# Kernel tuning notes

Measured on AMD Instinct MI355X. Metric: run time of the kernel, lower is better.

## Reference

```python
import jax, jax.numpy as jnp
import numpy as np

N_NODES = 50000


def gcn_layer(h, src, dst, W, b):
    # h: [N, Fin] -> [N, Fout]; symmetric-normalized aggregation with self-loops
    h = h @ W
    n = h.shape[0]
    deg = jnp.zeros((n,), h.dtype).at[dst].add(1.0) + 1.0  # +1 for self-loop
    dinv = jax.lax.rsqrt(deg)
    msg = h[src] * dinv[src, None]                      # gather + scale by src norm
    agg = jax.ops.segment_sum(msg, dst, num_segments=n) # scatter-add at dst
    agg = agg * dinv[:, None]                           # scale by dst norm
    agg = agg + h * (dinv * dinv)[:, None]              # self-loop contribution
    return agg + b


def setup_inputs() -> dict:
    key = jax.random.key(0)
    ks = jax.random.split(key, 8)
    G, N, E, F = 8, N_NODES, 800000, 128
    x = jax.random.normal(ks[0], (G, N, F), dtype=jnp.float32)
    edge_index = jax.random.randint(ks[1], (G, 2, E), 0, N, dtype=jnp.int64)
    s = 1.0 / np.sqrt(F)
    W0 = jax.random.normal(ks[2], (F, F), dtype=jnp.float32) * s
    W1 = jax.random.normal(ks[3], (F, F), dtype=jnp.float32) * s
    W2 = jax.random.normal(ks[4], (F, F), dtype=jnp.float32) * s
    b0 = jnp.zeros((F,), jnp.float32)
    b1 = jnp.zeros((F,), jnp.float32)
    b2 = jnp.zeros((F,), jnp.float32)
    return {"x": x, "edge_index": edge_index, "W0": W0, "b0": b0,
            "W1": W1, "b1": b1, "W2": W2, "b2": b2}


def reference(x, edge_index, W0, b0, W1, b1, W2, b2):
    # dropout is identity in eval mode; relu applied after every layer
    def per_graph(xg, eg):
        src, dst = eg[0], eg[1]
        h = xg
        for W, b in ((W0, b0), (W1, b1), (W2, b2)):
            h = jax.nn.relu(gcn_layer(h, src, dst, W, b))
        return h
    return jax.vmap(per_graph)(x, edge_index)  # [G, N, output_dim]
```

## Files before the change

### kernel.cpp

```cpp
#include <hip/hip_runtime.h>

constexpr int G    = 8;
constexpr int NN   = 50000;
constexpr int EE   = 800000;
constexpr int F    = 128;
constexpr int NBK  = (NN + 255) / 256;
constexpr int CAP2 = 4608;
constexpr int CHA  = 8192;
constexpr int NBA  = (EE + CHA - 1) / CHA;

typedef float  float4_t __attribute__((ext_vector_type(4)));
typedef float  f32x4    __attribute__((ext_vector_type(4)));
typedef __bf16 bf16x8   __attribute__((ext_vector_type(8)));
typedef unsigned short u16x4 __attribute__((ext_vector_type(4)));
typedef unsigned short u16x8 __attribute__((ext_vector_type(8)));
typedef int            i32x4 __attribute__((ext_vector_type(4)));

__device__ inline float bf2f(unsigned short u) {
  union { unsigned int i; float f; } v; v.i = (unsigned int)u << 16; return v.f;
}
__device__ inline unsigned short f2bf(float f) {
  union { __bf16 b; unsigned short u; } v; v.b = (__bf16)f; return v.u;
}
__device__ inline void addrow(f32x4& a, f32x4& b, u16x8 v) {
  a += (f32x4){bf2f(v[0]), bf2f(v[1]), bf2f(v[2]), bf2f(v[3])};
  b += (f32x4){bf2f(v[4]), bf2f(v[5]), bf2f(v[6]), bf2f(v[7])};
}


__global__ __launch_bounds__(256) void binA_kernel(const int* __restrict__ edges,
                                                   int* __restrict__ bcur,
                                                   unsigned int* __restrict__ tmp,
                                                   int gbase, int Cg) {
  __shared__ int hist[NBK];
  __shared__ int hbase[NBK];
  int bid = blockIdx.x;
  int gw = bid % Cg, cb = bid / Cg;
  size_t ebase = (size_t)(gbase + gw) * 2 * EE;
  const int* srcp = edges + ebase;
  const int* dstp = edges + ebase + EE;
  int t = threadIdx.x;
  for (int i = t; i < NBK; i += 256) hist[i] = 0;
  __syncthreads();
  int e0 = cb * CHA;
  #pragma unroll
  for (int p = 0; p < CHA / 1024; ++p) {
    int e = e0 + (p * 256 + t) * 4;
    if (e < EE) {
      i32x4 d4 = __builtin_nontemporal_load((const i32x4*)(dstp + e));
      atomicAdd(&hist[d4.x >> 8], 1);
      atomicAdd(&hist[d4.y >> 8], 1);
      atomicAdd(&hist[d4.z >> 8], 1);
      atomicAdd(&hist[d4.w >> 8], 1);
    }
  }
  __syncthreads();
  for (int i = t; i < NBK; i += 256) {
    int c = hist[i];
    hbase[i] = c ? atomicAdd(&bcur[gw * NBK + i], c) : 0;
    hist[i] = 0;
  }
  __syncthreads();
  unsigned int* tg = tmp + (size_t)gw * NBK * CAP2;
  #pragma unroll
  for (int p = 0; p < CHA / 1024; ++p) {
    int e = e0 + (p * 256 + t) * 4;
    if (e < EE) {
      i32x4 s4 = __builtin_nontemporal_load((const i32x4*)(srcp + e));
      i32x4 d4 = __builtin_nontemporal_load((const i32x4*)(dstp + e));
      int dd[4] = {d4.x, d4.y, d4.z, d4.w};
      int ss[4] = {s4.x, s4.y, s4.z, s4.w};
      #pragma unroll
      for (int j = 0; j < 4; ++j) {
        int b = dd[j] >> 8;
        int pos = hbase[b] + atomicAdd(&hist[b], 1);
        if (pos < CAP2)
          tg[(size_t)b * CAP2 + pos] = ((unsigned)(dd[j] & 255) << 16) | (unsigned)ss[j];
      }
    }
  }
}


__global__ __launch_bounds__(256) void bscan_kernel(const int* __restrict__ bcur,
                                                    int* __restrict__ bbase) {
  __shared__ int wsum[4];
  int gw = blockIdx.x;
  int t = threadIdx.x;
  int lane = t & 63, wid = t >> 6;
  int v = (t < NBK) ? bcur[gw * NBK + t] : 0;
  int incl = v;
  #pragma unroll
  for (int off = 1; off < 64; off <<= 1) {
    int x = __shfl_up(incl, off);
    if (lane >= off) incl += x;
  }
  if (lane == 63) wsum[wid] = incl;
  __syncthreads();
  if (t == 0) {
    int s = 0;
    for (int w = 0; w < 4; ++w) { int x = wsum[w]; wsum[w] = s; s += x; }
  }
  __syncthreads();
  if (t < NBK) bbase[gw * NBK + t] = wsum[wid] + incl - v;
}


__global__ __launch_bounds__(256) void binB_kernel(const unsigned int* __restrict__ tmp,
                                                   const int* __restrict__ bcur,
                                                   const int* __restrict__ bbase,
                                                   unsigned short* __restrict__ csr,
                                                   int* __restrict__ row_off,
                                                   float* __restrict__ dinv, int Cg) {
  __shared__ int cnt256[256];
  __shared__ int cur256[256];
  __shared__ int wsum[4];
  int bid = blockIdx.x;
  int gw = bid % Cg, b = bid / Cg;
  int t = threadIdx.x;
  int cnt = bcur[gw * NBK + b]; if (cnt > CAP2) cnt = CAP2;
  int bb = bbase[gw * NBK + b];
  const unsigned int* tg = tmp + ((size_t)gw * NBK + b) * CAP2;
  int n0 = b << 8;
  int nNode = NN - n0; if (nNode > 256) nNode = 256;
  cnt256[t] = 0;
  __syncthreads();
  for (int i = t; i < cnt; i += 256)
    atomicAdd(&cnt256[tg[i] >> 16], 1);
  __syncthreads();
  int v = cnt256[t];
  int lane = t & 63, wid = t >> 6;
  int incl = v;
  #pragma unroll
  for (int off = 1; off < 64; off <<= 1) {
    int x = __shfl_up(incl, off);
    if (lane >= off) incl += x;
  }
  if (lane == 63) wsum[wid] = incl;
  __syncthreads();
  if (t == 0) {
    int s = 0;
    for (int w = 0; w < 4; ++w) { int x = wsum[w]; wsum[w] = s; s += x; }
  }
  __syncthreads();
  int excl = wsum[wid] + incl - v;
  cur256[t] = excl;
  int* ro = row_off + gw * (NN + 1);
  if (t < nNode) {
    ro[n0 + t] = bb + excl;
    (dinv + (size_t)gw * NN)[n0 + t] = rsqrtf((float)v + 1.0f);
  }
  if (b == NBK - 1 && t == nNode) ro[NN] = bb + cnt;
  __syncthreads();
  unsigned short* cg = csr + (size_t)gw * EE;
  for (int i = t; i < cnt; i += 256) {
    unsigned int u = tg[i];
    int slot = atomicAdd(&cur256[u >> 16], 1);
    cg[bb + slot] = (unsigned short)(u & 0xffff);
  }
}


__global__ __launch_bounds__(256) void wtprep_kernel(const float* __restrict__ W0,
                                                     const float* __restrict__ W1,
                                                     const float* __restrict__ W2,
                                                     __bf16* __restrict__ wt) {
  const float* Wl[3] = {W0, W1, W2};
  int l = blockIdx.x;
  const float* W = Wl[l];
  __bf16* hi = wt + (size_t)l * 2 * F * F;
  __bf16* lo = hi + F * F;
  for (int idx = threadIdx.x; idx < F * F; idx += 256) {
    int k = idx >> 7, c = idx & 127;
    float f = W[idx];
    __bf16 h = (__bf16)f;
    hi[c * F + k] = h;
    lo[c * F + k] = (__bf16)(f - (float)h);
  }
}


template<int MODE>
__global__ __launch_bounds__(256) void gemm_kernel(const void* __restrict__ actp,
                                                   const __bf16* __restrict__ wt,
                                                   const float* __restrict__ dinv,
                                                   unsigned short* __restrict__ h1,
                                                   int gbase, int Cg) {
  int w = threadIdx.x >> 6, l = threadIdx.x & 63;
  int wave = blockIdx.x * 4 + w;
  int cg  = wave & 3;
  int i16 = l & 15, kq = l >> 4;

  bf16x8 Bhi[2][4], Blo[2][4];
  #pragma unroll
  for (int t2 = 0; t2 < 2; ++t2) {
    int col = cg * 32 + t2 * 16 + i16;
    #pragma unroll
    for (int ks = 0; ks < 4; ++ks) {
      Bhi[t2][ks] = *(const bf16x8*)(wt +         (size_t)col * F + ks * 32 + kq * 8);
      Blo[t2][ks] = *(const bf16x8*)(wt + F * F + (size_t)col * F + ks * 32 + kq * 8);
    }
  }

  int ntask = Cg * 3125 * 4;
  int stride = gridDim.x * 4;
  for (int task = wave; task < ntask; task += stride) {
    int chunk = task >> 2;
    int gw = chunk / 3125, ch = chunk - gw * 3125;
    int row = ch * 16 + i16;
    size_t rbase = (size_t)row * F + kq * 8;

    f32x4 acc0 = {0.f, 0.f, 0.f, 0.f}, acc1 = acc0;
    if (MODE == 0) {
      const float* ag = (const float*)actp + (size_t)(gbase + gw) * NN * F;
      #pragma unroll
      for (int ks = 0; ks < 4; ++ks) {
        float4_t v0 = *(const float4_t*)(ag + rbase + ks * 32);
        float4_t v1 = *(const float4_t*)(ag + rbase + ks * 32 + 4);
        bf16x8 ahi, alo;
        #pragma unroll
        for (int j = 0; j < 4; ++j) {
          __bf16 h0 = (__bf16)v0[j], h1v = (__bf16)v1[j];
          ahi[j] = h0;     ahi[j + 4] = h1v;
          alo[j] = (__bf16)(v0[j] - (float)h0);
          alo[j + 4] = (__bf16)(v1[j] - (float)h1v);
        }
        acc0 = __builtin_amdgcn_mfma_f32_16x16x32_bf16(Bhi[0][ks], ahi, acc0, 0, 0, 0);
        acc0 = __builtin_amdgcn_mfma_f32_16x16x32_bf16(Blo[0][ks], ahi, acc0, 0, 0, 0);
        acc0 = __builtin_amdgcn_mfma_f32_16x16x32_bf16(Bhi[0][ks], alo, acc0, 0, 0, 0);
        acc1 = __builtin_amdgcn_mfma_f32_16x16x32_bf16(Bhi[1][ks], ahi, acc1, 0, 0, 0);
        acc1 = __builtin_amdgcn_mfma_f32_16x16x32_bf16(Blo[1][ks], ahi, acc1, 0, 0, 0);
        acc1 = __builtin_amdgcn_mfma_f32_16x16x32_bf16(Bhi[1][ks], alo, acc1, 0, 0, 0);
      }
    } else {
      const unsigned short* ag = (const unsigned short*)actp + (size_t)gw * NN * F;
      #pragma unroll
      for (int ks = 0; ks < 4; ++ks) {
        bf16x8 a = *(const bf16x8*)((const __bf16*)ag + rbase + ks * 32);
        acc0 = __builtin_amdgcn_mfma_f32_16x16x32_bf16(Bhi[0][ks], a, acc0, 0, 0, 0);
        acc0 = __builtin_amdgcn_mfma_f32_16x16x32_bf16(Blo[0][ks], a, acc0, 0, 0, 0);
        acc1 = __builtin_amdgcn_mfma_f32_16x16x32_bf16(Bhi[1][ks], a, acc1, 0, 0, 0);
        acc1 = __builtin_amdgcn_mfma_f32_16x16x32_bf16(Blo[1][ks], a, acc1, 0, 0, 0);
      }
    }
    float di = (dinv + (size_t)gw * NN)[row];
    unsigned short* hr = h1 + (size_t)gw * NN * F + (size_t)row * F + cg * 32 + kq * 4;
    u16x4 o0, o1;
    #pragma unroll
    for (int q = 0; q < 4; ++q) { o0[q] = f2bf(acc0[q] * di); o1[q] = f2bf(acc1[q] * di); }
    *(u16x4*)hr = o0;
    *(u16x4*)(hr + 16) = o1;
  }
}


template<int FIN>
__global__ __launch_bounds__(256) void agg_kernel(const unsigned short* __restrict__ h1,
                                                  const unsigned short* __restrict__ csr,
                                                  const int* __restrict__ row_off,
                                                  const float* __restrict__ dinv,
                                                  const float* __restrict__ bias,
                                                  void* __restrict__ outp, int gbase, int Cg) {
  int bid = blockIdx.x;
  int gw = bid % Cg, xb = bid / Cg;
  const unsigned short* hg = h1 + (size_t)gw * NN * F;
  const unsigned short* cs = csr + (size_t)gw * EE;
  const int*   ro = row_off + gw * (NN + 1);
  const float* dv = dinv + (size_t)gw * NN;

  int grp = threadIdx.x >> 4, lane = threadIdx.x & 15;
  int node = xb * 16 + grp;
  int e0 = ro[node], e1 = ro[node + 1];
  float di = dv[node];
  f32x4 a0 = {0.f, 0.f, 0.f, 0.f}, b0 = a0, a1 = a0, b1 = a0;
  addrow(a0, b0, *(const u16x8*)(hg + (size_t)node * F + lane * 8));
  int e = e0;
  for (; e + 3 < e1; e += 4) {
    int s0 = cs[e], s1 = cs[e + 1], s2 = cs[e + 2], s3 = cs[e + 3];
    u16x8 v0 = *(const u16x8*)(hg + (size_t)s0 * F + lane * 8);
    u16x8 v1 = *(const u16x8*)(hg + (size_t)s1 * F + lane * 8);
    u16x8 v2 = *(const u16x8*)(hg + (size_t)s2 * F + lane * 8);
    u16x8 v3 = *(const u16x8*)(hg + (size_t)s3 * F + lane * 8);
    addrow(a0, b0, v0);
    addrow(a1, b1, v1);
    addrow(a0, b0, v2);
    addrow(a1, b1, v3);
  }
  for (; e < e1; ++e) {
    int s = cs[e];
    addrow(a0, b0, *(const u16x8*)(hg + (size_t)s * F + lane * 8));
  }
  f32x4 ra = a0 + a1, rb = b0 + b1;
  float4_t bb0 = *(const float4_t*)(bias + lane * 8);
  float4_t bb1 = *(const float4_t*)(bias + lane * 8 + 4);
  #pragma unroll
  for (int j = 0; j < 4; ++j) {
    ra[j] = fmaxf(fmaf(ra[j], di, bb0[j]), 0.f);
    rb[j] = fmaxf(fmaf(rb[j], di, bb1[j]), 0.f);
  }
  if (FIN) {
    float* og = (float*)outp + (size_t)(gbase + gw) * NN * F + (size_t)node * F + lane * 8;
    *(float4_t*)og = ra;
    *(float4_t*)(og + 4) = rb;
  } else {
    u16x8 o;
    #pragma unroll
    for (int j = 0; j < 4; ++j) { o[j] = f2bf(ra[j]); o[j + 4] = f2bf(rb[j]); }
    unsigned short* og = (unsigned short*)outp + (size_t)gw * NN * F + (size_t)node * F + lane * 8;
    *(u16x8*)og = o;
  }
}


extern "C" void kernel_launch(void* const* d_in, const int* in_sizes, int n_in,
                              void* d_out, int out_size, void* d_ws, size_t ws_size,
                              hipStream_t stream) {
  const float* x     = (const float*)d_in[0];
  const int*   edges = (const int*)d_in[1];
  const float* Ws[3] = {(const float*)d_in[2], (const float*)d_in[4], (const float*)d_in[6]};
  const float* bs[3] = {(const float*)d_in[3], (const float*)d_in[5], (const float*)d_in[7]};
  float* out = (float*)d_out;

  size_t sz_h1  = (size_t)NN * F * 2;
  size_t sz_wt  = (size_t)3 * 2 * F * F * 2;
  size_t sz_csr = (size_t)EE * 2;
  size_t sz_bk  = (size_t)NBK * 4;
  size_t sz_dv  = (size_t)NN * 4;
  size_t sz_ro  = (size_t)(NN + 1) * 4;
  size_t per_g  = 2 * sz_h1 + sz_csr + 2 * sz_bk + sz_dv + sz_ro;

  int CB = (int)((ws_size > sz_wt ? ws_size - sz_wt : 0) / per_g);
  if (CB < 1) CB = 1;
  if (CB > G) CB = G;

  char* p = (char*)d_ws;
  unsigned short* h1      = (unsigned short*)p;  p += sz_h1 * CB;
  unsigned short* actb    = (unsigned short*)p;  p += sz_h1 * CB;
  __bf16*         wt      = (__bf16*)p;          p += sz_wt;
  unsigned short* csr     = (unsigned short*)p;  p += sz_csr * CB;
  int*            bcur    = (int*)p;             p += sz_bk * CB;
  int*            bbase   = (int*)p;             p += sz_bk * CB;
  float*          dinv    = (float*)p;           p += sz_dv * CB;
  int*            row_off = (int*)p;

  wtprep_kernel<<<3, 256, 0, stream>>>(Ws[0], Ws[1], Ws[2], wt);

  int nblk_m = 2048;
  int nblk_a = NN / 16;

  for (int gb = 0; gb < G; gb += CB) {
    int Cg = G - gb < CB ? G - gb : CB;
    hipMemsetAsync(bcur, 0, sz_bk * Cg, stream);
    binA_kernel <<<NBA * Cg, 256, 0, stream>>>(edges, bcur, (unsigned int*)actb, gb, Cg);
    bscan_kernel<<<Cg, 256, 0, stream>>>(bcur, bbase);
    binB_kernel <<<NBK * Cg, 256, 0, stream>>>((const unsigned int*)actb, bcur, bbase,
                                               csr, row_off, dinv, Cg);

    gemm_kernel<0><<<nblk_m, 256, 0, stream>>>(x, wt, dinv, h1, gb, Cg);
    agg_kernel<0><<<nblk_a * Cg, 256, 0, stream>>>(h1, csr, row_off, dinv, bs[0], actb, gb, Cg);
    gemm_kernel<1><<<nblk_m, 256, 0, stream>>>(actb, wt + 2 * F * F, dinv, h1, gb, Cg);
    agg_kernel<0><<<nblk_a * Cg, 256, 0, stream>>>(h1, csr, row_off, dinv, bs[1], actb, gb, Cg);
    gemm_kernel<1><<<nblk_m, 256, 0, stream>>>(actb, wt + 4 * F * F, dinv, h1, gb, Cg);
    agg_kernel<1><<<nblk_a * Cg, 256, 0, stream>>>(h1, csr, row_off, dinv, bs[2], out, gb, Cg);
  }
}
```

Measured before the change: 998.2 us.

## Fuse aggregation with next layer's GEMM via LDS tile, ping-pong h1 buffers

Layers 1 and 2 now run in one kernel. It aggregates 64 nodes' neighbour rows into an LDS tile, applies bias and ReLU, then multiplies the tile by the next weight matrix with MFMA and writes the scaled bf16 result to an alternate buffer. This removes the intermediate activation write and re-read plus two kernel launches. The final aggregation uses nontemporal stores for the fp32 output. The trade-off is lower occupancy from the LDS tile and B-fragment registers, and a serialisation between the gather phase and the MFMA phase inside each block.

Result: slower. 1.081 ms (+8.3%).

```diff
diff --git a/kernel.cpp b/kernel.cpp
--- a/kernel.cpp
+++ b/kernel.cpp
@@ -180,12 +180,11 @@
 }
 
 
-template<int MODE>
-__global__ __launch_bounds__(256) void gemm_kernel(const void* __restrict__ actp,
-                                                   const __bf16* __restrict__ wt,
-                                                   const float* __restrict__ dinv,
-                                                   unsigned short* __restrict__ h1,
-                                                   int gbase, int Cg) {
+__global__ __launch_bounds__(256) void gemm0_kernel(const float* __restrict__ act,
+                                                    const __bf16* __restrict__ wt,
+                                                    const float* __restrict__ dinv,
+                                                    unsigned short* __restrict__ h1,
+                                                    int gbase, int Cg) {
   int w = threadIdx.x >> 6, l = threadIdx.x & 63;
   int wave = blockIdx.x * 4 + w;
   int cg  = wave & 3;
@@ -211,37 +210,25 @@
     size_t rbase = (size_t)row * F + kq * 8;
 
     f32x4 acc0 = {0.f, 0.f, 0.f, 0.f}, acc1 = acc0;
-    if (MODE == 0) {
-      const float* ag = (const float*)actp + (size_t)(gbase + gw) * NN * F;
+    const float* ag = (const float*)act + (size_t)(gbase + gw) * NN * F;
+    #pragma unroll
+    for (int ks = 0; ks < 4; ++ks) {
+      float4_t v0 = *(const float4_t*)(ag + rbase + ks * 32);
+      float4_t v1 = *(const float4_t*)(ag + rbase + ks * 32 + 4);
+      bf16x8 ahi, alo;
       #pragma unroll
-      for (int ks = 0; ks < 4; ++ks) {
-        float4_t v0 = *(const float4_t*)(ag + rbase + ks * 32);
-        float4_t v1 = *(const float4_t*)(ag + rbase + ks * 32 + 4);
-        bf16x8 ahi, alo;
-        #pragma unroll
-        for (int j = 0; j < 4; ++j) {
-          __bf16 h0 = (__bf16)v0[j], h1v = (__bf16)v1[j];
-          ahi[j] = h0;     ahi[j + 4] = h1v;
-          alo[j] = (__bf16)(v0[j] - (float)h0);
-          alo[j + 4] = (__bf16)(v1[j] - (float)h1v);
-        }
-        acc0 = __builtin_amdgcn_mfma_f32_16x16x32_bf16(Bhi[0][ks], ahi, acc0, 0, 0, 0);
-        acc0 = __builtin_amdgcn_mfma_f32_16x16x32_bf16(Blo[0][ks], ahi, acc0, 0, 0, 0);
-        acc0 = __builtin_amdgcn_mfma_f32_16x16x32_bf16(Bhi[0][ks], alo, acc0, 0, 0, 0);
-        acc1 = __builtin_amdgcn_mfma_f32_16x16x32_bf16(Bhi[1][ks], ahi, acc1, 0, 0, 0);
-        acc1 = __builtin_amdgcn_mfma_f32_16x16x32_bf16(Blo[1][ks], ahi, acc1, 0, 0, 0);
-        acc1 = __builtin_amdgcn_mfma_f32_16x16x32_bf16(Bhi[1][ks], alo, acc1, 0, 0, 0);
+      for (int j = 0; j < 4; ++j) {
+        __bf16 h0 = (__bf16)v0[j], h1v = (__bf16)v1[j];
+        ahi[j] = h0;     ahi[j + 4] = h1v;
+        alo[j] = (__bf16)(v0[j] - (float)h0);
+        alo[j + 4] = (__bf16)(v1[j] - (float)h1v);
       }
-    } else {
-      const unsigned short* ag = (const unsigned short*)actp + (size_t)gw * NN * F;
-      #pragma unroll
-      for (int ks = 0; ks < 4; ++ks) {
-        bf16x8 a = *(const bf16x8*)((const __bf16*)ag + rbase + ks * 32);
-        acc0 = __builtin_amdgcn_mfma_f32_16x16x32_bf16(Bhi[0][ks], a, acc0, 0, 0, 0);
-        acc0 = __builtin_amdgcn_mfma_f32_16x16x32_bf16(Blo[0][ks], a, acc0, 0, 0, 0);
-        acc1 = __builtin_amdgcn_mfma_f32_16x16x32_bf16(Bhi[1][ks], a, acc1, 0, 0, 0);
-        acc1 = __builtin_amdgcn_mfma_f32_16x16x32_bf16(Blo[1][ks], a, acc1, 0, 0, 0);
-      }
+      acc0 = __builtin_amdgcn_mfma_f32_16x16x32_bf16(Bhi[0][ks], ahi, acc0, 0, 0, 0);
+      acc0 = __builtin_amdgcn_mfma_f32_16x16x32_bf16(Blo[0][ks], ahi, acc0, 0, 0, 0);
+      acc0 = __builtin_amdgcn_mfma_f32_16x16x32_bf16(Bhi[0][ks], alo, acc0, 0, 0, 0);
+      acc1 = __builtin_amdgcn_mfma_f32_16x16x32_bf16(Bhi[1][ks], ahi, acc1, 0, 0, 0);
+      acc1 = __builtin_amdgcn_mfma_f32_16x16x32_bf16(Blo[1][ks], ahi, acc1, 0, 0, 0);
+      acc1 = __builtin_amdgcn_mfma_f32_16x16x32_bf16(Bhi[1][ks], alo, acc1, 0, 0, 0);
     }
     float di = (dinv + (size_t)gw * NN)[row];
     unsigned short* hr = h1 + (size_t)gw * NN * F + (size_t)row * F + cg * 32 + kq * 4;
@@ -254,13 +241,108 @@
 }
 
 
-template<int FIN>
-__global__ __launch_bounds__(256) void agg_kernel(const unsigned short* __restrict__ h1,
-                                                  const unsigned short* __restrict__ csr,
-                                                  const int* __restrict__ row_off,
-                                                  const float* __restrict__ dinv,
-                                                  const float* __restrict__ bias,
-                                                  void* __restrict__ outp, int gbase, int Cg) {
+__global__ __launch_bounds__(256) void fused_kernel(const unsigned short* __restrict__ h1src,
+                                                    const unsigned short* __restrict__ csr,
+                                                    const int* __restrict__ row_off,
+                                                    const float* __restrict__ dinv,
+                                                    const float* __restrict__ bias,
+                                                    const __bf16* __restrict__ wt,
+                                                    unsigned short* __restrict__ h1dst,
+                                                    int Cg) {
+  __shared__ unsigned short As[64][136];
+  int bid = blockIdx.x;
+  int gw = bid % Cg, xb = bid / Cg;
+  const unsigned short* hg = h1src + (size_t)gw * NN * F;
+  const unsigned short* cs = csr + (size_t)gw * EE;
+  const int*   ro = row_off + gw * (NN + 1);
+  const float* dv = dinv + (size_t)gw * NN;
+  int row0 = xb * 64;
+  int t = threadIdx.x;
+  int w = t >> 6, l = t & 63;
+  int i16 = l & 15, kq = l >> 4;
+
+  bf16x8 Bhi[2][4], Blo[2][4];
+  #pragma unroll
+  for (int t2 = 0; t2 < 2; ++t2) {
+    int col = w * 32 + t2 * 16 + i16;
+    #pragma unroll
+    for (int ks = 0; ks < 4; ++ks) {
+      Bhi[t2][ks] = *(const bf16x8*)(wt +         (size_t)col * F + ks * 32 + kq * 8);
+      Blo[t2][ks] = *(const bf16x8*)(wt + F * F + (size_t)col * F + ks * 32 + kq * 8);
+    }
+  }
+
+  int grp = t >> 4, lane = t & 15;
+  #pragma unroll
+  for (int pass = 0; pass < 4; ++pass) {
+    int r = pass * 16 + grp;
+    int node = row0 + r;
+    u16x8 o = (u16x8){0, 0, 0, 0, 0, 0, 0, 0};
+    if (node < NN) {
+      int e0 = ro[node], e1 = ro[node + 1];
+      float di = dv[node];
+      f32x4 a0 = {0.f, 0.f, 0.f, 0.f}, b0 = a0, a1 = a0, b1 = a0;
+      addrow(a0, b0, *(const u16x8*)(hg + (size_t)node * F + lane * 8));
+      int e = e0;
+      for (; e + 3 < e1; e += 4) {
+        int s0 = cs[e], s1 = cs[e + 1], s2 = cs[e + 2], s3 = cs[e + 3];
+        u16x8 v0 = *(const u16x8*)(hg + (size_t)s0 * F + lane * 8);
+        u16x8 v1 = *(const u16x8*)(hg + (size_t)s1 * F + lane * 8);
+        u16x8 v2 = *(const u16x8*)(hg + (size_t)s2 * F + lane * 8);
+        u16x8 v3 = *(const u16x8*)(hg + (size_t)s3 * F + lane * 8);
+        addrow(a0, b0, v0);
+        addrow(a1, b1, v1);
+        addrow(a0, b0, v2);
+        addrow(a1, b1, v3);
+      }
+      for (; e < e1; ++e) {
+        int s = cs[e];
+        addrow(a0, b0, *(const u16x8*)(hg + (size_t)s * F + lane * 8));
+      }
+      f32x4 ra = a0 + a1, rb = b0 + b1;
+      float4_t bb0 = *(const float4_t*)(bias + lane * 8);
+      float4_t bb1 = *(const float4_t*)(bias + lane * 8 + 4);
+      #pragma unroll
+      for (int j = 0; j < 4; ++j) {
+        o[j]     = f2bf(fmaxf(fmaf(ra[j], di, bb0[j]), 0.f));
+        o[j + 4] = f2bf(fmaxf(fmaf(rb[j], di, bb1[j]), 0.f));
+      }
+    }
+    *(u16x8*)(&As[r][lane * 8]) = o;
+  }
+  __syncthreads();
+
+  #pragma unroll
+  for (int rt = 0; rt < 4; ++rt) {
+    int row = row0 + rt * 16 + i16;
+    f32x4 acc0 = {0.f, 0.f, 0.f, 0.f}, acc1 = acc0;
+    #pragma unroll
+    for (int ks = 0; ks < 4; ++ks) {
+      bf16x8 a = *(const bf16x8*)((const __bf16*)&As[rt * 16 + i16][ks * 32 + kq * 8]);
+      acc0 = __builtin_amdgcn_mfma_f32_16x16x32_bf16(Bhi[0][ks], a, acc0, 0, 0, 0);
+      acc0 = __builtin_amdgcn_mfma_f32_16x16x32_bf16(Blo[0][ks], a, acc0, 0, 0, 0);
+      acc1 = __builtin_amdgcn_mfma_f32_16x16x32_bf16(Bhi[1][ks], a, acc1, 0, 0, 0);
+      acc1 = __builtin_amdgcn_mfma_f32_16x16x32_bf16(Blo[1][ks], a, acc1, 0, 0, 0);
+    }
+    if (row < NN) {
+      float di = dv[row];
+      unsigned short* hr = h1dst + (size_t)gw * NN * F + (size_t)row * F + w * 32 + kq * 4;
+      u16x4 o0, o1;
+      #pragma unroll
+      for (int q = 0; q < 4; ++q) { o0[q] = f2bf(acc0[q] * di); o1[q] = f2bf(acc1[q] * di); }
+      *(u16x4*)hr = o0;
+      *(u16x4*)(hr + 16) = o1;
+    }
+  }
+}
+
+
+__global__ __launch_bounds__(256) void aggf_kernel(const unsigned short* __restrict__ h1,
+                                                   const unsigned short* __restrict__ csr,
+                                                   const int* __restrict__ row_off,
+                                                   const float* __restrict__ dinv,
+                                                   const float* __restrict__ bias,
+                                                   float* __restrict__ out, int gbase, int Cg) {
   int bid = blockIdx.x;
   int gw = bid % Cg, xb = bid / Cg;
   const unsigned short* hg = h1 + (size_t)gw * NN * F;
@@ -298,17 +380,9 @@
     ra[j] = fmaxf(fmaf(ra[j], di, bb0[j]), 0.f);
     rb[j] = fmaxf(fmaf(rb[j], di, bb1[j]), 0.f);
   }
-  if (FIN) {
-    float* og = (float*)outp + (size_t)(gbase + gw) * NN * F + (size_t)node * F + lane * 8;
-    *(float4_t*)og = ra;
-    *(float4_t*)(og + 4) = rb;
-  } else {
-    u16x8 o;
-    #pragma unroll
-    for (int j = 0; j < 4; ++j) { o[j] = f2bf(ra[j]); o[j + 4] = f2bf(rb[j]); }
-    unsigned short* og = (unsigned short*)outp + (size_t)gw * NN * F + (size_t)node * F + lane * 8;
-    *(u16x8*)og = o;
-  }
+  float* og = out + (size_t)(gbase + gw) * NN * F + (size_t)node * F + lane * 8;
+  __builtin_nontemporal_store(ra, (f32x4*)og);
+  __builtin_nontemporal_store(rb, (f32x4*)(og + 4));
 }
 
 
@@ -334,8 +408,8 @@
   if (CB > G) CB = G;
 
   char* p = (char*)d_ws;
-  unsigned short* h1      = (unsigned short*)p;  p += sz_h1 * CB;
-  unsigned short* actb    = (unsigned short*)p;  p += sz_h1 * CB;
+  unsigned short* h1a     = (unsigned short*)p;  p += sz_h1 * CB;
+  unsigned short* h1b     = (unsigned short*)p;  p += sz_h1 * CB;
   __bf16*         wt      = (__bf16*)p;          p += sz_wt;
   unsigned short* csr     = (unsigned short*)p;  p += sz_csr * CB;
   int*            bcur    = (int*)p;             p += sz_bk * CB;
@@ -346,21 +420,22 @@
   wtprep_kernel<<<3, 256, 0, stream>>>(Ws[0], Ws[1], Ws[2], wt);
 
   int nblk_m = 2048;
+  int nblk_f = (NN + 63) / 64;
   int nblk_a = NN / 16;
 
   for (int gb = 0; gb < G; gb += CB) {
     int Cg = G - gb < CB ? G - gb : CB;
     hipMemsetAsync(bcur, 0, sz_bk * Cg, stream);
-    binA_kernel <<<NBA * Cg, 256, 0, stream>>>(edges, bcur, (unsigned int*)actb, gb, Cg);
+    binA_kernel <<<NBA * Cg, 256, 0, stream>>>(edges, bcur, (unsigned int*)h1b, gb, Cg);
     bscan_kernel<<<Cg, 256, 0, stream>>>(bcur, bbase);
-    binB_kernel <<<NBK * Cg, 256, 0, stream>>>((const unsigned int*)actb, bcur, bbase,
+    binB_kernel <<<NBK * Cg, 256, 0, stream>>>((const unsigned int*)h1b, bcur, bbase,
                                                csr, row_off, dinv, Cg);
 
-    gemm_kernel<0><<<nblk_m, 256, 0, stream>>>(x, wt, dinv, h1, gb, Cg);
-    agg_kernel<0><<<nblk_a * Cg, 256, 0, stream>>>(h1, csr, row_off, dinv, bs[0], actb, gb, Cg);
-    gemm_kernel<1><<<nblk_m, 256, 0, stream>>>(actb, wt + 2 * F * F, dinv, h1, gb, Cg);
-    agg_kernel<0><<<nblk_a * Cg, 256, 0, stream>>>(h1, csr, row_off, dinv, bs[1], actb, gb, Cg);
-    gemm_kernel<1><<<nblk_m, 256, 0, stream>>>(actb, wt + 4 * F * F, dinv, h1, gb, Cg);
-    agg_kernel<1><<<nblk_a * Cg, 256, 0, stream>>>(h1, csr, row_off, dinv, bs[2], out, gb, Cg);
-  }
-}
+    gemm0_kernel<<<nblk_m, 256, 0, stream>>>(x, wt, dinv, h1a, gb, Cg);
+    fused_kernel<<<nblk_f * Cg, 256, 0, stream>>>(h1a, csr, row_off, dinv, bs[0],
+                                                  wt + 2 * F * F, h1b, Cg);
+    fused_kernel<<<nblk_f * Cg, 256, 0, stream>>>(h1b, csr, row_off, dinv, bs[1],
+                                                  wt + 4 * F * F, h1a, Cg);
+    aggf_kernel<<<nblk_a * Cg, 256, 0, stream>>>(h1a, csr, row_off, dinv, bs[2], out, gb, Cg);
+  }
+}
```

## Split aggregation into four feature-quarter passes for better cache locality

Applied to the files above, without the earlier changes.

The aggregation kernel now runs as four launches, each covering a 32-column slice of the 128 features, with 4 lanes per node and 64 nodes per block. The gathered working set per pass is a quarter of the feature matrix, so random neighbor gathers are more likely to hit in L2/MALL. CSR index loads and output stores are switched to nontemporal hints to keep them from polluting cache. In exchange, the CSR indices and row offsets are re-read four times and there are more kernel launches.

After: 1.436 ms. +43.9%, slower.

```diff
diff --git a/kernel.cpp b/kernel.cpp
--- a/kernel.cpp
+++ b/kernel.cpp
@@ -260,23 +260,28 @@
                                                   const int* __restrict__ row_off,
                                                   const float* __restrict__ dinv,
                                                   const float* __restrict__ bias,
-                                                  void* __restrict__ outp, int gbase, int Cg) {
+                                                  void* __restrict__ outp, int gbase, int Cg,
+                                                  int q) {
   int bid = blockIdx.x;
   int gw = bid % Cg, xb = bid / Cg;
-  const unsigned short* hg = h1 + (size_t)gw * NN * F;
+  const unsigned short* hg = h1 + (size_t)gw * NN * F + q * 32;
   const unsigned short* cs = csr + (size_t)gw * EE;
   const int*   ro = row_off + gw * (NN + 1);
   const float* dv = dinv + (size_t)gw * NN;
 
-  int grp = threadIdx.x >> 4, lane = threadIdx.x & 15;
-  int node = xb * 16 + grp;
+  int grp = threadIdx.x >> 2, lane = threadIdx.x & 3;
+  int node = xb * 64 + grp;
+  if (node >= NN) return;
   int e0 = ro[node], e1 = ro[node + 1];
   float di = dv[node];
   f32x4 a0 = {0.f, 0.f, 0.f, 0.f}, b0 = a0, a1 = a0, b1 = a0;
   addrow(a0, b0, *(const u16x8*)(hg + (size_t)node * F + lane * 8));
   int e = e0;
   for (; e + 3 < e1; e += 4) {
-    int s0 = cs[e], s1 = cs[e + 1], s2 = cs[e + 2], s3 = cs[e + 3];
+    int s0 = (int)__builtin_nontemporal_load(cs + e);
+    int s1 = (int)__builtin_nontemporal_load(cs + e + 1);
+    int s2 = (int)__builtin_nontemporal_load(cs + e + 2);
+    int s3 = (int)__builtin_nontemporal_load(cs + e + 3);
     u16x8 v0 = *(const u16x8*)(hg + (size_t)s0 * F + lane * 8);
     u16x8 v1 = *(const u16x8*)(hg + (size_t)s1 * F + lane * 8);
     u16x8 v2 = *(const u16x8*)(hg + (size_t)s2 * F + lane * 8);
@@ -287,27 +292,28 @@
     addrow(a1, b1, v3);
   }
   for (; e < e1; ++e) {
-    int s = cs[e];
+    int s = (int)__builtin_nontemporal_load(cs + e);
     addrow(a0, b0, *(const u16x8*)(hg + (size_t)s * F + lane * 8));
   }
   f32x4 ra = a0 + a1, rb = b0 + b1;
-  float4_t bb0 = *(const float4_t*)(bias + lane * 8);
-  float4_t bb1 = *(const float4_t*)(bias + lane * 8 + 4);
+  const float* bq = bias + q * 32;
+  float4_t bb0 = *(const float4_t*)(bq + lane * 8);
+  float4_t bb1 = *(const float4_t*)(bq + lane * 8 + 4);
   #pragma unroll
   for (int j = 0; j < 4; ++j) {
     ra[j] = fmaxf(fmaf(ra[j], di, bb0[j]), 0.f);
     rb[j] = fmaxf(fmaf(rb[j], di, bb1[j]), 0.f);
   }
   if (FIN) {
-    float* og = (float*)outp + (size_t)(gbase + gw) * NN * F + (size_t)node * F + lane * 8;
-    *(float4_t*)og = ra;
-    *(float4_t*)(og + 4) = rb;
+    float* og = (float*)outp + (size_t)(gbase + gw) * NN * F + (size_t)node * F + q * 32 + lane * 8;
+    __builtin_nontemporal_store(ra, (f32x4*)og);
+    __builtin_nontemporal_store(rb, (f32x4*)(og + 4));
   } else {
     u16x8 o;
     #pragma unroll
     for (int j = 0; j < 4; ++j) { o[j] = f2bf(ra[j]); o[j + 4] = f2bf(rb[j]); }
-    unsigned short* og = (unsigned short*)outp + (size_t)gw * NN * F + (size_t)node * F + lane * 8;
-    *(u16x8*)og = o;
+    unsigned short* og = (unsigned short*)outp + (size_t)gw * NN * F + (size_t)node * F + q * 32 + lane * 8;
+    __builtin_nontemporal_store(o, (u16x8*)og);
   }
 }
 
@@ -346,7 +352,7 @@
   wtprep_kernel<<<3, 256, 0, stream>>>(Ws[0], Ws[1], Ws[2], wt);
 
   int nblk_m = 2048;
-  int nblk_a = NN / 16;
+  int nblk_q = (NN + 63) / 64;
 
   for (int gb = 0; gb < G; gb += CB) {
     int Cg = G - gb < CB ? G - gb : CB;
@@ -356,11 +362,21 @@
     binB_kernel <<<NBK * Cg, 256, 0, stream>>>((const unsigned int*)actb, bcur, bbase,
                                                csr, row_off, dinv, Cg);
 
-    gemm_kernel<0><<<nblk_m, 256, 0, stream>>>(x, wt, dinv, h1, gb, Cg);
-    agg_kernel<0><<<nblk_a * Cg, 256, 0, stream>>>(h1, csr, row_off, dinv, bs[0], actb, gb, Cg);
-    gemm_kernel<1><<<nblk_m, 256, 0, stream>>>(actb, wt + 2 * F * F, dinv, h1, gb, Cg);
-    agg_kernel<0><<<nblk_a * Cg, 256, 0, stream>>>(h1, csr, row_off, dinv, bs[1], actb, gb, Cg);
-    gemm_kernel<1><<<nblk_m, 256, 0, stream>>>(actb, wt + 4 * F * F, dinv, h1, gb, Cg);
-    agg_kernel<1><<<nblk_a * Cg, 256, 0, stream>>>(h1, csr, row_off, dinv, bs[2], out, gb, Cg);
-  }
-}
+    for (int l = 0; l < 3; ++l) {
+      if (l == 0)
+        gemm_kernel<0><<<nblk_m, 256, 0, stream>>>(x, wt, dinv, h1, gb, Cg);
+      else
+        gemm_kernel<1><<<nblk_m, 256, 0, stream>>>(actb, wt + (size_t)l * 2 * F * F,
+                                                   dinv, h1, gb, Cg);
+      if (l < 2) {
+        for (int q = 0; q < 4; ++q)
+          agg_kernel<0><<<nblk_q * Cg, 256, 0, stream>>>(h1, csr, row_off, dinv, bs[l],
+                                                         actb, gb, Cg, q);
+      } else {
+        for (int q = 0; q < 4; ++q)
+          agg_kernel<1><<<nblk_q * Cg, 256, 0, stream>>>(h1, csr, row_off, dinv, bs[l],
+                                                         out, gb, Cg, q);
+      }
+    }
+  }
+}
```

## Stage GEMM activation tiles in LDS so each row is loaded once per block

Applied to the files above, without the earlier changes.

The persistent GEMM had each of four column-group waves reload the same 16-row activation slice from global memory. The new kernels launch one block per 64-row tile and load that tile into LDS once with coalesced vector loads. All four waves then read it from LDS, each covering 32 output columns. The final fp32 output is also written with nontemporal stores. The cost is a larger grid with per-block weight-fragment reloads and LDS use that may lower occupancy.

Measured after the change: 964.8 us. 1.03x faster.

```diff
diff --git a/kernel.cpp b/kernel.cpp
--- a/kernel.cpp
+++ b/kernel.cpp
@@ -180,21 +180,25 @@
 }
 
 
-template<int MODE>
-__global__ __launch_bounds__(256) void gemm_kernel(const void* __restrict__ actp,
-                                                   const __bf16* __restrict__ wt,
-                                                   const float* __restrict__ dinv,
-                                                   unsigned short* __restrict__ h1,
-                                                   int gbase, int Cg) {
-  int w = threadIdx.x >> 6, l = threadIdx.x & 63;
-  int wave = blockIdx.x * 4 + w;
-  int cg  = wave & 3;
+__global__ __launch_bounds__(256) void gemm0_kernel(const float* __restrict__ act,
+                                                    const __bf16* __restrict__ wt,
+                                                    const float* __restrict__ dinv,
+                                                    unsigned short* __restrict__ h1,
+                                                    int gbase, int Cg) {
+  __shared__ float As[64][132];
+  int bid = blockIdx.x;
+  int gw = bid % Cg, xb = bid / Cg;
+  const float* ag = act + (size_t)(gbase + gw) * NN * F;
+  const float* dv = dinv + (size_t)gw * NN;
+  int row0 = xb * 64;
+  int t = threadIdx.x;
+  int w = t >> 6, l = t & 63;
   int i16 = l & 15, kq = l >> 4;
 
   bf16x8 Bhi[2][4], Blo[2][4];
   #pragma unroll
   for (int t2 = 0; t2 < 2; ++t2) {
-    int col = cg * 32 + t2 * 16 + i16;
+    int col = w * 32 + t2 * 16 + i16;
     #pragma unroll
     for (int ks = 0; ks < 4; ++ks) {
       Bhi[t2][ks] = *(const bf16x8*)(wt +         (size_t)col * F + ks * 32 + kq * 8);
@@ -202,54 +206,113 @@
     }
   }
 
-  int ntask = Cg * 3125 * 4;
-  int stride = gridDim.x * 4;
-  for (int task = wave; task < ntask; task += stride) {
-    int chunk = task >> 2;
-    int gw = chunk / 3125, ch = chunk - gw * 3125;
-    int row = ch * 16 + i16;
-    size_t rbase = (size_t)row * F + kq * 8;
-
+  #pragma unroll
+  for (int p = 0; p < 8; ++p) {
+    int idx = p * 256 + t;
+    int r = idx >> 5, c = (idx & 31) * 4;
+    int grow = row0 + r;
+    float4_t v = {0.f, 0.f, 0.f, 0.f};
+    if (grow < NN) v = *(const float4_t*)(ag + (size_t)grow * F + c);
+    *(float4_t*)(&As[r][c]) = v;
+  }
+  __syncthreads();
+
+  #pragma unroll
+  for (int rt = 0; rt < 4; ++rt) {
+    int arow = rt * 16 + i16;
     f32x4 acc0 = {0.f, 0.f, 0.f, 0.f}, acc1 = acc0;
-    if (MODE == 0) {
-      const float* ag = (const float*)actp + (size_t)(gbase + gw) * NN * F;
+    #pragma unroll
+    for (int ks = 0; ks < 4; ++ks) {
+      float4_t v0 = *(const float4_t*)(&As[arow][ks * 32 + kq * 8]);
+      float4_t v1 = *(const float4_t*)(&As[arow][ks * 32 + kq * 8 + 4]);
+      bf16x8 ahi, alo;
       #pragma unroll
-      for (int ks = 0; ks < 4; ++ks) {
-        float4_t v0 = *(const float4_t*)(ag + rbase + ks * 32);
-        float4_t v1 = *(const float4_t*)(ag + rbase + ks * 32 + 4);
-        bf16x8 ahi, alo;
-        #pragma unroll
-        for (int j = 0; j < 4; ++j) {
-          __bf16 h0 = (__bf16)v0[j], h1v = (__bf16)v1[j];
-          ahi[j] = h0;     ahi[j + 4] = h1v;
-          alo[j] = (__bf16)(v0[j] - (float)h0);
-          alo[j + 4] = (__bf16)(v1[j] - (float)h1v);
-        }
-        acc0 = __builtin_amdgcn_mfma_f32_16x16x32_bf16(Bhi[0][ks], ahi, acc0, 0, 0, 0);
-        acc0 = __builtin_amdgcn_mfma_f32_16x16x32_bf16(Blo[0][ks], ahi, acc0, 0, 0, 0);
-        acc0 = __builtin_amdgcn_mfma_f32_16x16x32_bf16(Bhi[0][ks], alo, acc0, 0, 0, 0);
-        acc1 = __builtin_amdgcn_mfma_f32_16x16x32_bf16(Bhi[1][ks], ahi, acc1, 0, 0, 0);
-        acc1 = __builtin_amdgcn_mfma_f32_16x16x32_bf16(Blo[1][ks], ahi, acc1, 0, 0, 0);
-        acc1 = __builtin_amdgcn_mfma_f32_16x16x32_bf16(Bhi[1][ks], alo, acc1, 0, 0, 0);
+      for (int j = 0; j < 4; ++j) {
+        __bf16 h0 = (__bf16)v0[j], h1v = (__bf16)v1[j];
+        ahi[j] = h0;     ahi[j + 4] = h1v;
+        alo[j] = (__bf16)(v0[j] - (float)h0);
+        alo[j + 4] = (__bf16)(v1[j] - (float)h1v);
       }
-    } else {
-      const unsigned short* ag = (const unsigned short*)actp + (size_t)gw * NN * F;
+      acc0 = __builtin_amdgcn_mfma_f32_16x16x32_bf16(Bhi[0][ks], ahi, acc0, 0, 0, 0);
+      acc0 = __builtin_amdgcn_mfma_f32_16x16x32_bf16(Blo[0][ks], ahi, acc0, 0, 0, 0);
+      acc0 = __builtin_amdgcn_mfma_f32_16x16x32_bf16(Bhi[0][ks], alo, acc0, 0, 0, 0);
+      acc1 = __builtin_amdgcn_mfma_f32_16x16x32_bf16(Bhi[1][ks], ahi, acc1, 0, 0, 0);
+      acc1 = __builtin_amdgcn_mfma_f32_16x16x32_bf16(Blo[1][ks], ahi, acc1, 0, 0, 0);
+      acc1 = __builtin_amdgcn_mfma_f32_16x16x32_bf16(Bhi[1][ks], alo, acc1, 0, 0, 0);
+    }
+    int row = row0 + arow;
+    if (row < NN) {
+      float di = dv[row];
+      unsigned short* hr = h1 + (size_t)gw * NN * F + (size_t)row * F + w * 32 + kq * 4;
+      u16x4 o0, o1;
       #pragma unroll
-      for (int ks = 0; ks < 4; ++ks) {
-        bf16x8 a = *(const bf16x8*)((const __bf16*)ag + rbase + ks * 32);
-        acc0 = __builtin_amdgcn_mfma_f32_16x16x32_bf16(Bhi[0][ks], a, acc0, 0, 0, 0);
-        acc0 = __builtin_amdgcn_mfma_f32_16x16x32_bf16(Blo[0][ks], a, acc0, 0, 0, 0);
-        acc1 = __builtin_amdgcn_mfma_f32_16x16x32_bf16(Bhi[1][ks], a, acc1, 0, 0, 0);
-        acc1 = __builtin_amdgcn_mfma_f32_16x16x32_bf16(Blo[1][ks], a, acc1, 0, 0, 0);
-      }
-    }
-    float di = (dinv + (size_t)gw * NN)[row];
-    unsigned short* hr = h1 + (size_t)gw * NN * F + (size_t)row * F + cg * 32 + kq * 4;
-    u16x4 o0, o1;
+      for (int q = 0; q < 4; ++q) { o0[q] = f2bf(acc0[q] * di); o1[q] = f2bf(acc1[q] * di); }
+      *(u16x4*)hr = o0;
+      *(u16x4*)(hr + 16) = o1;
+    }
+  }
+}
+
+
+__global__ __launch_bounds__(256) void gemm1_kernel(const unsigned short* __restrict__ actb,
+                                                    const __bf16* __restrict__ wt,
+                                                    const float* __restrict__ dinv,
+                                                    unsigned short* __restrict__ h1,
+                                                    int Cg) {
+  __shared__ unsigned short As[64][136];
+  int bid = blockIdx.x;
+  int gw = bid % Cg, xb = bid / Cg;
+  const unsigned short* ag = actb + (size_t)gw * NN * F;
+  const float* dv = dinv + (size_t)gw * NN;
+  int row0 = xb * 64;
+  int t = threadIdx.x;
+  int w = t >> 6, l = t & 63;
+  int i16 = l & 15, kq = l >> 4;
+
+  bf16x8 Bhi[2][4], Blo[2][4];
+  #pragma unroll
+  for (int t2 = 0; t2 < 2; ++t2) {
+    int col = w * 32 + t2 * 16 + i16;
     #pragma unroll
-    for (int q = 0; q < 4; ++q) { o0[q] = f2bf(acc0[q] * di); o1[q] = f2bf(acc1[q] * di); }
-    *(u16x4*)hr = o0;
-    *(u16x4*)(hr + 16) = o1;
+    for (int ks = 0; ks < 4; ++ks) {
+      Bhi[t2][ks] = *(const bf16x8*)(wt +         (size_t)col * F + ks * 32 + kq * 8);
+      Blo[t2][ks] = *(const bf16x8*)(wt + F * F + (size_t)col * F + ks * 32 + kq * 8);
+    }
+  }
+
+  #pragma unroll
+  for (int p = 0; p < 4; ++p) {
+    int idx = p * 256 + t;
+    int r = idx >> 4, c = (idx & 15) * 8;
+    int grow = row0 + r;
+    u16x8 v = (u16x8){0, 0, 0, 0, 0, 0, 0, 0};
+    if (grow < NN) v = *(const u16x8*)(ag + (size_t)grow * F + c);
+    *(u16x8*)(&As[r][c]) = v;
+  }
+  __syncthreads();
+
+  #pragma unroll
+  for (int rt = 0; rt < 4; ++rt) {
+    int arow = rt * 16 + i16;
+    f32x4 acc0 = {0.f, 0.f, 0.f, 0.f}, acc1 = acc0;
+    #pragma unroll
+    for (int ks = 0; ks < 4; ++ks) {
+      bf16x8 a = *(const bf16x8*)((const __bf16*)&As[arow][ks * 32 + kq * 8]);
+      acc0 = __builtin_amdgcn_mfma_f32_16x16x32_bf16(Bhi[0][ks], a, acc0, 0, 0, 0);
+      acc0 = __builtin_amdgcn_mfma_f32_16x16x32_bf16(Blo[0][ks], a, acc0, 0, 0, 0);
+      acc1 = __builtin_amdgcn_mfma_f32_16x16x32_bf16(Bhi[1][ks], a, acc1, 0, 0, 0);
+      acc1 = __builtin_amdgcn_mfma_f32_16x16x32_bf16(Blo[1][ks], a, acc1, 0, 0, 0);
+    }
+    int row = row0 + arow;
+    if (row < NN) {
+      float di = dv[row];
+      unsigned short* hr = h1 + (size_t)gw * NN * F + (size_t)row * F + w * 32 + kq * 4;
+      u16x4 o0, o1;
+      #pragma unroll
+      for (int q = 0; q < 4; ++q) { o0[q] = f2bf(acc0[q] * di); o1[q] = f2bf(acc1[q] * di); }
+      *(u16x4*)hr = o0;
+      *(u16x4*)(hr + 16) = o1;
+    }
   }
 }
 
@@ -300,8 +363,8 @@
   }
   if (FIN) {
     float* og = (float*)outp + (size_t)(gbase + gw) * NN * F + (size_t)node * F + lane * 8;
-    *(float4_t*)og = ra;
-    *(float4_t*)(og + 4) = rb;
+    __builtin_nontemporal_store(ra, (f32x4*)og);
+    __builtin_nontemporal_store(rb, (f32x4*)(og + 4));
   } else {
     u16x8 o;
     #pragma unroll
@@ -345,7 +408,7 @@
 
   wtprep_kernel<<<3, 256, 0, stream>>>(Ws[0], Ws[1], Ws[2], wt);
 
-  int nblk_m = 2048;
+  int nblk_g = (NN + 63) / 64;
   int nblk_a = NN / 16;
 
   for (int gb = 0; gb < G; gb += CB) {
@@ -356,11 +419,11 @@
     binB_kernel <<<NBK * Cg, 256, 0, stream>>>((const unsigned int*)actb, bcur, bbase,
                                                csr, row_off, dinv, Cg);
 
-    gemm_kernel<0><<<nblk_m, 256, 0, stream>>>(x, wt, dinv, h1, gb, Cg);
+    gemm0_kernel<<<nblk_g * Cg, 256, 0, stream>>>(x, wt, dinv, h1, gb, Cg);
     agg_kernel<0><<<nblk_a * Cg, 256, 0, stream>>>(h1, csr, row_off, dinv, bs[0], actb, gb, Cg);
-    gemm_kernel<1><<<nblk_m, 256, 0, stream>>>(actb, wt + 2 * F * F, dinv, h1, gb, Cg);
+    gemm1_kernel<<<nblk_g * Cg, 256, 0, stream>>>(actb, wt + 2 * F * F, dinv, h1, Cg);
     agg_kernel<0><<<nblk_a * Cg, 256, 0, stream>>>(h1, csr, row_off, dinv, bs[1], actb, gb, Cg);
-    gemm_kernel<1><<<nblk_m, 256, 0, stream>>>(actb, wt + 4 * F * F, dinv, h1, gb, Cg);
+    gemm1_kernel<<<nblk_g * Cg, 256, 0, stream>>>(actb, wt + 4 * F * F, dinv, h1, Cg);
     agg_kernel<1><<<nblk_a * Cg, 256, 0, stream>>>(h1, csr, row_off, dinv, bs[2], out, gb, Cg);
   }
 }
```
